# Kernel optimization log

Hardware: AMD Instinct MI355X
Metric: run time of the kernel (lower is better)

The kernel has to match this reference:

```python
import jax, jax.numpy as jnp
import numpy as np

K_MSG = 1024   # message length k (rows of G)
N_CODE = 2048  # codeword length n (cols of G)
B = 32768      # number of message blocks


def setup_inputs() -> dict:
    key = jax.random.key(0)
    kb, kg = jax.random.split(key)
    b = jax.random.randint(kb, (B, K_MSG), 0, 2, dtype=jnp.int32)
    G = jax.random.randint(kg, (K_MSG, N_CODE), 0, 2, dtype=jnp.int32)
    return {"b": b, "G": G}


def reference(b, G):
    # GF(2) linear block encode: c = (b @ G) mod 2
    # b: [num_blocks, k] bits (0/1), G: [k, n] generator matrix (0/1)
    b2 = b.astype(jnp.int32)
    G2 = G.astype(jnp.int32)
    c = jnp.mod(jnp.matmul(b2, G2), 2)  # [num_blocks, n]
    return c.astype(jnp.int32)
```

## Files before the change

### kernel.cpp

```cpp
#include <hip/hip_runtime.h>
#include <stdint.h>

typedef unsigned int u32;
typedef int v4i  __attribute__((ext_vector_type(4)));
typedef int v16i __attribute__((ext_vector_type(16)));

#define K_MSG   1024
#define N_CODE  2048
#define NB      32768

__global__ void pack_bi8(const int* __restrict__ b, u32* __restrict__ bi8) {
    const int nthr = gridDim.x * blockDim.x;
    int idx = blockIdx.x * blockDim.x + threadIdx.x;
    const int ndw = NB * K_MSG / 4;
    for (; idx < ndw; idx += nthr) {
        int4 v = *(const int4*)(b + (size_t)idx * 4);
        bi8[idx] = (u32)(v.x & 1) | ((u32)(v.y & 1) << 8) |
                   ((u32)(v.z & 1) << 16) | ((u32)(v.w & 1) << 24);
    }
}

__global__ void pack_gBF(const int* __restrict__ G, u32* __restrict__ bf) {
    int idx = blockIdx.x * blockDim.x + threadIdx.x;
    const int j  = idx & (N_CODE - 1);
    const int kq = idx >> 11;
    u32 p = 0;
#pragma unroll
    for (int i = 0; i < 4; ++i) {
        int v = G[(size_t)(kq * 4 + i) * N_CODE + j];
        p |= (u32)(v & 1) << (8 * i);
    }
    const int jb = j >> 5, jr = j & 31;
    const int kb = kq >> 3, hi = (kq >> 2) & 1, b4 = kq & 3;
    bf[(size_t)(jb * 32 + kb) * 256 + hi * 128 + jr * 4 + b4] = p;
}


#define MFMA_SET(sfx) do {                                                         \
    acc[0][0] = __builtin_amdgcn_mfma_i32_32x32x32_i8(a0##sfx, b0##sfx, acc[0][0], 0,0,0); \
    acc[0][1] = __builtin_amdgcn_mfma_i32_32x32x32_i8(a0##sfx, b1##sfx, acc[0][1], 0,0,0); \
    acc[0][2] = __builtin_amdgcn_mfma_i32_32x32x32_i8(a0##sfx, b2##sfx, acc[0][2], 0,0,0); \
    acc[0][3] = __builtin_amdgcn_mfma_i32_32x32x32_i8(a0##sfx, b3##sfx, acc[0][3], 0,0,0); \
    acc[1][0] = __builtin_amdgcn_mfma_i32_32x32x32_i8(a1##sfx, b0##sfx, acc[1][0], 0,0,0); \
    acc[1][1] = __builtin_amdgcn_mfma_i32_32x32x32_i8(a1##sfx, b1##sfx, acc[1][1], 0,0,0); \
    acc[1][2] = __builtin_amdgcn_mfma_i32_32x32x32_i8(a1##sfx, b2##sfx, acc[1][2], 0,0,0); \
    acc[1][3] = __builtin_amdgcn_mfma_i32_32x32x32_i8(a1##sfx, b3##sfx, acc[1][3], 0,0,0); \
} while (0)

#define LOAD_SET(sfx, s_) do {                                                     \
    int ao_ = lr * 1024 + ((((s_) * 32) + hi * 16) ^ axor);                        \
    a0##sfx = *(const v4i*)(As + ao_);                                             \
    a1##sfx = *(const v4i*)(As + ao_ + 32768);                                     \
    b0##sfx = *(const v4i*)(bp0 + (size_t)(s_) * 1024);                            \
    b1##sfx = *(const v4i*)(bp1 + (size_t)(s_) * 1024);                            \
    b2##sfx = *(const v4i*)(bp2 + (size_t)(s_) * 1024);                            \
    b3##sfx = *(const v4i*)(bp3 + (size_t)(s_) * 1024);                            \
} while (0)

__global__ __launch_bounds__(256, 2) void gemm_i8(const char* __restrict__ bi8,
                                                  const char* __restrict__ bf,
                                                  int* __restrict__ out) {
    __shared__ __align__(16) char As[64 * 1024];

    const int t   = threadIdx.x;
    const int bid = blockIdx.x;
    const int swz = (bid & 7) * 256 + (bid >> 3);
    const int m0  = (swz >> 2) * 64;
    const int n0  = (swz & 3) * 512;

    const int w  = t >> 6, lane = t & 63, lr = lane & 31, hi = lane >> 5;

    {
        const char* src = bi8 + (size_t)m0 * 1024;
#pragma unroll
        for (int i = 0; i < 16; ++i) {
            uint4 v = *(const uint4*)(src + i * 4096 + t * 16);
            int row = i * 4 + (t >> 6);
            int off = (t & 63) * 16;
            *(uint4*)(As + row * 1024 + (off ^ ((row & 7) << 4))) = v;
        }
    }
    __syncthreads();

    const char* bp0 = bf + ((size_t)(n0 >> 5) + w * 4) * 32768 + lane * 16;
    const char* bp1 = bp0 + 32768;
    const char* bp2 = bp0 + 65536;
    const char* bp3 = bp0 + 98304;
    const int axor = (lr & 7) << 4;

    v16i acc[2][4] = {};
    v4i a0A, a1A, b0A, b1A, b2A, b3A;
    v4i a0B, a1B, b0B, b1B, b2B, b3B;
    v4i a0C, a1C, b0C, b1C, b2C, b3C;
    v4i a0D, a1D, b0D, b1D, b2D, b3D;

    LOAD_SET(A, 0);
    LOAD_SET(B, 1);
#pragma unroll 1
    for (int s = 0; s < 32; s += 4) {
        LOAD_SET(C, s + 2);
        LOAD_SET(D, s + 3);
        MFMA_SET(A);
        MFMA_SET(B);
        if (s + 4 < 32) {
            LOAD_SET(A, s + 4);
            LOAD_SET(B, s + 5);
        }
        MFMA_SET(C);
        MFMA_SET(D);
    }

#pragma unroll
    for (int mi = 0; mi < 2; ++mi) {
#pragma unroll
        for (int ni = 0; ni < 4; ++ni) {
            const int cbase = n0 + w * 128 + ni * 32 + lr;
            const int rbase = m0 + mi * 32 + 4 * hi;
#pragma unroll
            for (int r = 0; r < 16; ++r) {
                const int row = rbase + (r & 3) + 8 * (r >> 2);
                out[(size_t)row * N_CODE + cbase] = acc[mi][ni][r] & 1;
            }
        }
    }
}

__global__ void encode_naive(const int* __restrict__ b, const int* __restrict__ G,
                             int* __restrict__ out) {
    size_t idx = (size_t)blockIdx.x * blockDim.x + threadIdx.x;
    size_t total = (size_t)NB * N_CODE;
    if (idx >= total) return;
    int i = (int)(idx / N_CODE);
    int j = (int)(idx % N_CODE);
    int acc = 0;
    for (int k = 0; k < K_MSG; ++k)
        acc ^= b[(size_t)i * K_MSG + k] & G[(size_t)k * N_CODE + j];
    out[idx] = acc & 1;
}

extern "C" void kernel_launch(void* const* d_in, const int* in_sizes, int n_in,
                              void* d_out, int out_size, void* d_ws, size_t ws_size,
                              hipStream_t stream) {
    const int* b = (const int*)d_in[0];
    const int* G = (const int*)d_in[1];
    int* out = (int*)d_out;

    const size_t bi8_bytes = (size_t)NB * K_MSG;
    const size_t bf_bytes  = (size_t)N_CODE * K_MSG;

    if (ws_size < bi8_bytes + bf_bytes) {
        size_t total = (size_t)NB * N_CODE;
        encode_naive<<<(unsigned)((total + 255) / 256), 256, 0, stream>>>(b, G, out);
        return;
    }

    char* bi8 = (char*)d_ws;
    char* bf  = (char*)d_ws + bi8_bytes;

    pack_bi8<<<2048, 256, 0, stream>>>(b, (u32*)bi8);
    pack_gBF<<<2048, 256, 0, stream>>>(G, (u32*)bf);

    gemm_i8<<<2048, 256, 0, stream>>>(bi8, bf, out);
}
```

Measured before the change: 150.1 us.

## Retile GEMM to 128x256 blocks with two-phase K staging of A

Changes the block tile from 64 rows x 512 cols to 128 rows x 256 cols, so each wave covers 4 M-subtiles by 2 N-subtiles and streams fewer B fragments per MFMA. The A tile (128 rows x full K) is staged into the same 64KB LDS in two K-halves with a barrier between phases. The aim is to cut global traffic for the packed generator matrix per unit of work and to shift more operand loads to LDS. In exchange it adds a mid-kernel sync and reload, and the load pipeline becomes shallower (two B sets instead of four), which may expose more load latency.

```diff
diff --git a/kernel.cpp b/kernel.cpp
--- a/kernel.cpp
+++ b/kernel.cpp
@@ -36,85 +36,89 @@
 }
 
 
-#define MFMA_SET(sfx) do {                                                         \
-    acc[0][0] = __builtin_amdgcn_mfma_i32_32x32x32_i8(a0##sfx, b0##sfx, acc[0][0], 0,0,0); \
-    acc[0][1] = __builtin_amdgcn_mfma_i32_32x32x32_i8(a0##sfx, b1##sfx, acc[0][1], 0,0,0); \
-    acc[0][2] = __builtin_amdgcn_mfma_i32_32x32x32_i8(a0##sfx, b2##sfx, acc[0][2], 0,0,0); \
-    acc[0][3] = __builtin_amdgcn_mfma_i32_32x32x32_i8(a0##sfx, b3##sfx, acc[0][3], 0,0,0); \
-    acc[1][0] = __builtin_amdgcn_mfma_i32_32x32x32_i8(a1##sfx, b0##sfx, acc[1][0], 0,0,0); \
-    acc[1][1] = __builtin_amdgcn_mfma_i32_32x32x32_i8(a1##sfx, b1##sfx, acc[1][1], 0,0,0); \
-    acc[1][2] = __builtin_amdgcn_mfma_i32_32x32x32_i8(a1##sfx, b2##sfx, acc[1][2], 0,0,0); \
-    acc[1][3] = __builtin_amdgcn_mfma_i32_32x32x32_i8(a1##sfx, b3##sfx, acc[1][3], 0,0,0); \
+#define MFMA_I8(va, vb, vc) __builtin_amdgcn_mfma_i32_32x32x32_i8(va, vb, vc, 0, 0, 0)
+
+#define MFMA_SET(sfx) do {                       \
+    acc[0][0] = MFMA_I8(a0, b0##sfx, acc[0][0]); \
+    acc[0][1] = MFMA_I8(a0, b1##sfx, acc[0][1]); \
+    acc[1][0] = MFMA_I8(a1, b0##sfx, acc[1][0]); \
+    acc[1][1] = MFMA_I8(a1, b1##sfx, acc[1][1]); \
+    acc[2][0] = MFMA_I8(a2, b0##sfx, acc[2][0]); \
+    acc[2][1] = MFMA_I8(a2, b1##sfx, acc[2][1]); \
+    acc[3][0] = MFMA_I8(a3, b0##sfx, acc[3][0]); \
+    acc[3][1] = MFMA_I8(a3, b1##sfx, acc[3][1]); \
 } while (0)
 
-#define LOAD_SET(sfx, s_) do {                                                     \
-    int ao_ = lr * 1024 + ((((s_) * 32) + hi * 16) ^ axor);                        \
-    a0##sfx = *(const v4i*)(As + ao_);                                             \
-    a1##sfx = *(const v4i*)(As + ao_ + 32768);                                     \
-    b0##sfx = *(const v4i*)(bp0 + (size_t)(s_) * 1024);                            \
-    b1##sfx = *(const v4i*)(bp1 + (size_t)(s_) * 1024);                            \
-    b2##sfx = *(const v4i*)(bp2 + (size_t)(s_) * 1024);                            \
-    b3##sfx = *(const v4i*)(bp3 + (size_t)(s_) * 1024);                            \
+#define LDA(s_)                                                \
+    const int ao_ = (((s_) * 32) + hi * 16) ^ axor;            \
+    v4i a0 = *(const v4i*)(As + (lr      ) * 512 + ao_);       \
+    v4i a1 = *(const v4i*)(As + (lr +  32) * 512 + ao_);       \
+    v4i a2 = *(const v4i*)(As + (lr +  64) * 512 + ao_);       \
+    v4i a3 = *(const v4i*)(As + (lr +  96) * 512 + ao_);
+
+#define LOADB(sfx, s_) do {                                    \
+    b0##sfx = *(const v4i*)(bp0 + (size_t)(s_) * 1024);        \
+    b1##sfx = *(const v4i*)(bp1 + (size_t)(s_) * 1024);        \
 } while (0)
 
 __global__ __launch_bounds__(256, 2) void gemm_i8(const char* __restrict__ bi8,
                                                   const char* __restrict__ bf,
                                                   int* __restrict__ out) {
-    __shared__ __align__(16) char As[64 * 1024];
+    __shared__ __align__(16) char As[128 * 512];
 
     const int t   = threadIdx.x;
     const int bid = blockIdx.x;
     const int swz = (bid & 7) * 256 + (bid >> 3);
-    const int m0  = (swz >> 2) * 64;
-    const int n0  = (swz & 3) * 512;
+    const int m0  = (swz >> 3) * 128;
+    const int n0  = (swz & 7) * 256;
 
-    const int w  = t >> 6, lane = t & 63, lr = lane & 31, hi = lane >> 5;
+    const int w = t >> 6, lane = t & 63, lr = lane & 31, hi = lane >> 5;
+    const int strow = t >> 1, sc = t & 1;
+    const int axor  = (lr & 7) << 4;
 
-    {
-        const char* src = bi8 + (size_t)m0 * 1024;
+    const char* bp0 = bf + ((size_t)(n0 >> 5) + w * 2) * 32768 + lane * 16;
+    const char* bp1 = bp0 + 32768;
+
+    const char* asrc = bi8 + (size_t)(m0 + strow) * 1024 + sc * 256;
+    char* adst = As + strow * 512;
+    const int dxor = (strow & 7) << 4;
+
+    v16i acc[4][2] = {};
+    v4i b0A, b1A, b0B, b1B;
+
+#pragma unroll 1
+    for (int ph = 0; ph < 2; ++ph) {
+        if (ph) __syncthreads();
 #pragma unroll
         for (int i = 0; i < 16; ++i) {
-            uint4 v = *(const uint4*)(src + i * 4096 + t * 16);
-            int row = i * 4 + (t >> 6);
-            int off = (t & 63) * 16;
-            *(uint4*)(As + row * 1024 + (off ^ ((row & 7) << 4))) = v;
+            uint4 v = *(const uint4*)(asrc + ph * 512 + i * 16);
+            *(uint4*)(adst + ((sc * 256 + i * 16) ^ dxor)) = v;
         }
-    }
-    __syncthreads();
+        __syncthreads();
 
-    const char* bp0 = bf + ((size_t)(n0 >> 5) + w * 4) * 32768 + lane * 16;
-    const char* bp1 = bp0 + 32768;
-    const char* bp2 = bp0 + 65536;
-    const char* bp3 = bp0 + 98304;
-    const int axor = (lr & 7) << 4;
-
-    v16i acc[2][4] = {};
-    v4i a0A, a1A, b0A, b1A, b2A, b3A;
-    v4i a0B, a1B, b0B, b1B, b2B, b3B;
-    v4i a0C, a1C, b0C, b1C, b2C, b3C;
-    v4i a0D, a1D, b0D, b1D, b2D, b3D;
-
-    LOAD_SET(A, 0);
-    LOAD_SET(B, 1);
+        const int kb = ph * 16;
+        LOADB(A, kb + 0);
+        LOADB(B, kb + 1);
 #pragma unroll 1
-    for (int s = 0; s < 32; s += 4) {
-        LOAD_SET(C, s + 2);
-        LOAD_SET(D, s + 3);
-        MFMA_SET(A);
-        MFMA_SET(B);
-        if (s + 4 < 32) {
-            LOAD_SET(A, s + 4);
-            LOAD_SET(B, s + 5);
+        for (int sl = 0; sl < 16; sl += 2) {
+            {
+                LDA(sl)
+                MFMA_SET(A);
+                if (sl + 2 < 16) LOADB(A, kb + sl + 2);
+            }
+            {
+                LDA(sl + 1)
+                MFMA_SET(B);
+                if (sl + 3 < 16) LOADB(B, kb + sl + 3);
+            }
         }
-        MFMA_SET(C);
-        MFMA_SET(D);
     }
 
 #pragma unroll
-    for (int mi = 0; mi < 2; ++mi) {
+    for (int mi = 0; mi < 4; ++mi) {
 #pragma unroll
-        for (int ni = 0; ni < 4; ++ni) {
-            const int cbase = n0 + w * 128 + ni * 32 + lr;
+        for (int ni = 0; ni < 2; ++ni) {
+            const int cbase = n0 + w * 64 + ni * 32 + lr;
             const int rbase = m0 + mi * 32 + 4 * hi;
 #pragma unroll
             for (int r = 0; r < 16; ++r) {
```

Measured after the change: 159.0 us. 1.06x slower.

## Fuse message bit packing into GEMM and loop all N passes per block

Applied to the files above, without the earlier changes.

Drops the separate pack_bi8 kernel and its 32 MB int8 intermediate. The GEMM block now reads int32 message bits directly, packs them to int8 in LDS, and loops over all four 512-column passes so each b row tile is loaded once. This removes a kernel launch and a full write and re-read of the packed buffer. In exchange the grid shrinks to 512 blocks with four serial passes each, which lowers parallelism, and the old block-index swizzle is gone.

```diff
diff --git a/kernel.cpp b/kernel.cpp
--- a/kernel.cpp
+++ b/kernel.cpp
@@ -8,17 +8,6 @@
 #define K_MSG   1024
 #define N_CODE  2048
 #define NB      32768
-
-__global__ void pack_bi8(const int* __restrict__ b, u32* __restrict__ bi8) {
-    const int nthr = gridDim.x * blockDim.x;
-    int idx = blockIdx.x * blockDim.x + threadIdx.x;
-    const int ndw = NB * K_MSG / 4;
-    for (; idx < ndw; idx += nthr) {
-        int4 v = *(const int4*)(b + (size_t)idx * 4);
-        bi8[idx] = (u32)(v.x & 1) | ((u32)(v.y & 1) << 8) |
-                   ((u32)(v.z & 1) << 16) | ((u32)(v.w & 1) << 24);
-    }
-}
 
 __global__ void pack_gBF(const int* __restrict__ G, u32* __restrict__ bf) {
     int idx = blockIdx.x * blockDim.x + threadIdx.x;
@@ -36,90 +25,91 @@
 }
 
 
-#define MFMA_SET(sfx) do {                                                         \
-    acc[0][0] = __builtin_amdgcn_mfma_i32_32x32x32_i8(a0##sfx, b0##sfx, acc[0][0], 0,0,0); \
-    acc[0][1] = __builtin_amdgcn_mfma_i32_32x32x32_i8(a0##sfx, b1##sfx, acc[0][1], 0,0,0); \
-    acc[0][2] = __builtin_amdgcn_mfma_i32_32x32x32_i8(a0##sfx, b2##sfx, acc[0][2], 0,0,0); \
-    acc[0][3] = __builtin_amdgcn_mfma_i32_32x32x32_i8(a0##sfx, b3##sfx, acc[0][3], 0,0,0); \
-    acc[1][0] = __builtin_amdgcn_mfma_i32_32x32x32_i8(a1##sfx, b0##sfx, acc[1][0], 0,0,0); \
-    acc[1][1] = __builtin_amdgcn_mfma_i32_32x32x32_i8(a1##sfx, b1##sfx, acc[1][1], 0,0,0); \
-    acc[1][2] = __builtin_amdgcn_mfma_i32_32x32x32_i8(a1##sfx, b2##sfx, acc[1][2], 0,0,0); \
-    acc[1][3] = __builtin_amdgcn_mfma_i32_32x32x32_i8(a1##sfx, b3##sfx, acc[1][3], 0,0,0); \
+#define MFMA_I8(va, vb, vc) __builtin_amdgcn_mfma_i32_32x32x32_i8(va, vb, vc, 0, 0, 0)
+
+#define MFMA_SET(sfx) do {                              \
+    acc[0][0] = MFMA_I8(a0##sfx, b0##sfx, acc[0][0]);   \
+    acc[0][1] = MFMA_I8(a0##sfx, b1##sfx, acc[0][1]);   \
+    acc[0][2] = MFMA_I8(a0##sfx, b2##sfx, acc[0][2]);   \
+    acc[0][3] = MFMA_I8(a0##sfx, b3##sfx, acc[0][3]);   \
+    acc[1][0] = MFMA_I8(a1##sfx, b0##sfx, acc[1][0]);   \
+    acc[1][1] = MFMA_I8(a1##sfx, b1##sfx, acc[1][1]);   \
+    acc[1][2] = MFMA_I8(a1##sfx, b2##sfx, acc[1][2]);   \
+    acc[1][3] = MFMA_I8(a1##sfx, b3##sfx, acc[1][3]);   \
 } while (0)
 
-#define LOAD_SET(sfx, s_) do {                                                     \
-    int ao_ = lr * 1024 + ((((s_) * 32) + hi * 16) ^ axor);                        \
-    a0##sfx = *(const v4i*)(As + ao_);                                             \
-    a1##sfx = *(const v4i*)(As + ao_ + 32768);                                     \
-    b0##sfx = *(const v4i*)(bp0 + (size_t)(s_) * 1024);                            \
-    b1##sfx = *(const v4i*)(bp1 + (size_t)(s_) * 1024);                            \
-    b2##sfx = *(const v4i*)(bp2 + (size_t)(s_) * 1024);                            \
-    b3##sfx = *(const v4i*)(bp3 + (size_t)(s_) * 1024);                            \
+#define LOAD_SET(sfx, s_) do {                                      \
+    int ao_ = lr * 1024 + ((((s_) * 32) + hi * 16) ^ axor);         \
+    a0##sfx = *(const v4i*)(As + ao_);                              \
+    a1##sfx = *(const v4i*)(As + ao_ + 32768);                      \
+    b0##sfx = *(const v4i*)(bp0 + (size_t)(s_) * 1024);             \
+    b1##sfx = *(const v4i*)(bp1 + (size_t)(s_) * 1024);             \
+    b2##sfx = *(const v4i*)(bp2 + (size_t)(s_) * 1024);             \
+    b3##sfx = *(const v4i*)(bp3 + (size_t)(s_) * 1024);             \
 } while (0)
 
-__global__ __launch_bounds__(256, 2) void gemm_i8(const char* __restrict__ bi8,
-                                                  const char* __restrict__ bf,
-                                                  int* __restrict__ out) {
+__global__ __launch_bounds__(256, 2) void gemm_fused(const int* __restrict__ b,
+                                                     const char* __restrict__ bf,
+                                                     int* __restrict__ out) {
     __shared__ __align__(16) char As[64 * 1024];
 
-    const int t   = threadIdx.x;
-    const int bid = blockIdx.x;
-    const int swz = (bid & 7) * 256 + (bid >> 3);
-    const int m0  = (swz >> 2) * 64;
-    const int n0  = (swz & 3) * 512;
-
-    const int w  = t >> 6, lane = t & 63, lr = lane & 31, hi = lane >> 5;
+    const int t  = threadIdx.x;
+    const int m0 = blockIdx.x * 64;
+    const int w = t >> 6, lane = t & 63, lr = lane & 31, hi = lane >> 5;
+    const int axor = (lr & 7) << 4;
 
     {
-        const char* src = bi8 + (size_t)m0 * 1024;
-#pragma unroll
-        for (int i = 0; i < 16; ++i) {
-            uint4 v = *(const uint4*)(src + i * 4096 + t * 16);
-            int row = i * 4 + (t >> 6);
-            int off = (t & 63) * 16;
-            *(uint4*)(As + row * 1024 + (off ^ ((row & 7) << 4))) = v;
+        const int* src = b + (size_t)m0 * K_MSG;
+#pragma unroll 8
+        for (int i = 0; i < 64; ++i) {
+            int4 v = *(const int4*)(src + (size_t)i * K_MSG + t * 4);
+            u32 p = (u32)(v.x & 1) | ((u32)(v.y & 1) << 8) |
+                    ((u32)(v.z & 1) << 16) | ((u32)(v.w & 1) << 24);
+            *(u32*)(As + i * 1024 + ((t * 4) ^ ((i & 7) << 4))) = p;
         }
     }
     __syncthreads();
 
-    const char* bp0 = bf + ((size_t)(n0 >> 5) + w * 4) * 32768 + lane * 16;
-    const char* bp1 = bp0 + 32768;
-    const char* bp2 = bp0 + 65536;
-    const char* bp3 = bp0 + 98304;
-    const int axor = (lr & 7) << 4;
+#pragma unroll 1
+    for (int pass = 0; pass < 4; ++pass) {
+        const char* bp0 = bf + ((size_t)pass * 16 + w * 4) * 32768 + lane * 16;
+        const char* bp1 = bp0 + 32768;
+        const char* bp2 = bp0 + 65536;
+        const char* bp3 = bp0 + 98304;
 
-    v16i acc[2][4] = {};
-    v4i a0A, a1A, b0A, b1A, b2A, b3A;
-    v4i a0B, a1B, b0B, b1B, b2B, b3B;
-    v4i a0C, a1C, b0C, b1C, b2C, b3C;
-    v4i a0D, a1D, b0D, b1D, b2D, b3D;
+        v16i acc[2][4] = {};
+        v4i a0A, a1A, b0A, b1A, b2A, b3A;
+        v4i a0B, a1B, b0B, b1B, b2B, b3B;
+        v4i a0C, a1C, b0C, b1C, b2C, b3C;
+        v4i a0D, a1D, b0D, b1D, b2D, b3D;
 
-    LOAD_SET(A, 0);
-    LOAD_SET(B, 1);
+        LOAD_SET(A, 0);
+        LOAD_SET(B, 1);
 #pragma unroll 1
-    for (int s = 0; s < 32; s += 4) {
-        LOAD_SET(C, s + 2);
-        LOAD_SET(D, s + 3);
-        MFMA_SET(A);
-        MFMA_SET(B);
-        if (s + 4 < 32) {
-            LOAD_SET(A, s + 4);
-            LOAD_SET(B, s + 5);
+        for (int s = 0; s < 32; s += 4) {
+            LOAD_SET(C, s + 2);
+            LOAD_SET(D, s + 3);
+            MFMA_SET(A);
+            MFMA_SET(B);
+            if (s + 4 < 32) {
+                LOAD_SET(A, s + 4);
+                LOAD_SET(B, s + 5);
+            }
+            MFMA_SET(C);
+            MFMA_SET(D);
         }
-        MFMA_SET(C);
-        MFMA_SET(D);
-    }
 
 #pragma unroll
-    for (int mi = 0; mi < 2; ++mi) {
+        for (int mi = 0; mi < 2; ++mi) {
 #pragma unroll
-        for (int ni = 0; ni < 4; ++ni) {
-            const int cbase = n0 + w * 128 + ni * 32 + lr;
-            const int rbase = m0 + mi * 32 + 4 * hi;
+            for (int ni = 0; ni < 4; ++ni) {
+                const int cbase = pass * 512 + w * 128 + ni * 32 + lr;
+                const int rbase = m0 + mi * 32 + 4 * hi;
 #pragma unroll
-            for (int r = 0; r < 16; ++r) {
-                const int row = rbase + (r & 3) + 8 * (r >> 2);
-                out[(size_t)row * N_CODE + cbase] = acc[mi][ni][r] & 1;
+                for (int r = 0; r < 16; ++r) {
+                    const int row = rbase + (r & 3) + 8 * (r >> 2);
+                    out[(size_t)row * N_CODE + cbase] = acc[mi][ni][r] & 1;
+                }
             }
         }
     }
@@ -145,20 +135,16 @@
     const int* G = (const int*)d_in[1];
     int* out = (int*)d_out;
 
-    const size_t bi8_bytes = (size_t)NB * K_MSG;
-    const size_t bf_bytes  = (size_t)N_CODE * K_MSG;
+    const size_t bf_bytes = (size_t)N_CODE * K_MSG;
 
-    if (ws_size < bi8_bytes + bf_bytes) {
+    if (ws_size < bf_bytes) {
         size_t total = (size_t)NB * N_CODE;
         encode_naive<<<(unsigned)((total + 255) / 256), 256, 0, stream>>>(b, G, out);
         return;
     }
 
-    char* bi8 = (char*)d_ws;
-    char* bf  = (char*)d_ws + bi8_bytes;
+    char* bf = (char*)d_ws;
 
-    pack_bi8<<<2048, 256, 0, stream>>>(b, (u32*)bi8);
     pack_gBF<<<2048, 256, 0, stream>>>(G, (u32*)bf);
-
-    gemm_i8<<<2048, 256, 0, stream>>>(bi8, bf, out);
+    gemm_fused<<<NB / 64, 256, 0, stream>>>(b, bf, out);
 }
```

New measurement: 166.5 us. 1.11x slower.
